# Kernel optimization log

Measured on AMD Instinct MI355X. Metric: run time of the kernel, lower is better.

The kernel has to match this reference:

```python
import jax, jax.numpy as jnp
import numpy as np

N, D = 16384, 16     # nodes (hits), node feature dim (= embedding dim, slice is full)
K = 64               # max_num_neighbors
MAX_RADIUS = 6.0     # kNN radius cut
PID_MAX = 5000


def setup_inputs() -> dict:
    key = jax.random.key(0)
    k1, k2 = jax.random.split(key)
    x = jax.random.normal(k1, (N, D), dtype=jnp.float32)
    particle_id = jax.random.randint(k2, (N,), 0, PID_MAX, dtype=jnp.int32)
    return {"x": x, "particle_id": particle_id}


def reference(x, particle_id):
    # ml is None and embedding_slice=(None,None) -> embedding features are x itself
    emb = x
    # knn_graph: squared pairwise distances, self-loops excluded (diag = +inf)
    sq = jnp.sum(emb * emb, axis=1)                       # [N]
    d2 = sq[:, None] + sq[None, :] - 2.0 * (emb @ emb.T)  # [N, N]
    diag = jnp.arange(N)
    d2 = d2.at[diag, diag].set(jnp.inf)
    _, nbr = jax.lax.top_k(-d2, K)                        # [N, K] nearest neighbor ids
    src = nbr.reshape(-1)                                 # edge_index[0]: neighbor (source)
    dst = jnp.repeat(jnp.arange(N, dtype=src.dtype), K)   # edge_index[1]: query node
    # radius filter: keep edges with dist < max_radius (fixed shape -> boolean mask)
    diff = x[src] - x[dst]                                # [N*K, D]
    dists = jnp.sqrt(jnp.maximum(jnp.sum(diff * diff, axis=1), 0.0))
    mask = dists < MAX_RADIUS                             # [N*K]
    # edge truth labels: same (nonzero) particle id on both ends
    y = (particle_id[src] == particle_id[dst]) & (particle_id[src] > 0) & mask
    # edge features: [x_src - x_dst, x_src + x_dst], zeroed on masked-out edges
    edge_features = jnp.concatenate([diff, x[src] + x[dst]], axis=1)
    edge_features = edge_features * mask[:, None].astype(x.dtype)
    edge_index = jnp.stack([src, dst])                    # [2, N*K]
    return x, edge_index, y.astype(jnp.int32), edge_features, mask
```

## Files before the change

kernel.cpp:

```cpp
#include <hip/hip_runtime.h>

#define NN 16384
#define DD 16
#define KK 64
#define QQ 4
#define TPB 256
#define HIST 1024
#define HISTW (HIST/2)
#define LIST_MAX 768
#define CAND_MAX 256

__device__ __forceinline__ float halving_sumsq16(const float* v) {
    float p[16];
#pragma unroll
    for (int d = 0; d < 16; ++d) p[d] = __fmul_rn(v[d], v[d]);
    float r8[8];
#pragma unroll
    for (int j = 0; j < 8; ++j) r8[j] = __fadd_rn(p[j], p[j + 8]);
    float r4[4];
#pragma unroll
    for (int j = 0; j < 4; ++j) r4[j] = __fadd_rn(r8[j], r8[j + 4]);
    float r2[2];
#pragma unroll
    for (int j = 0; j < 2; ++j) r2[j] = __fadd_rn(r4[j], r4[j + 2]);
    return __fadd_rn(r2[0], r2[1]);
}

__device__ __forceinline__ float d2_of(const float* xi, const float* xj,
                                       float sqi, float sqj) {
    float dot = 0.0f;
#pragma unroll
    for (int d = 0; d < DD; ++d) dot = fmaf(xi[d], xj[d], dot);
    return __fsub_rn(__fadd_rn(sqi, sqj), __fmul_rn(2.0f, dot));
}

__device__ __forceinline__ int bucket_of(float d2) {
    int b = (int)__fmul_rn(d2, 4.0f);
    if (b < 0) b = 0;
    if (b >= HIST) b = HIST - 1;
    return b;
}

#define LOAD_XQ()                                                              \
    float xq[QQ][DD];                                                          \
    float sq[QQ], Tq[QQ];                                                      \
    _Pragma("unroll") for (int q = 0; q < QQ; ++q) {                           \
        const float4* p = reinterpret_cast<const float4*>(x + (iA + q) * DD);  \
        float4 a0 = p[0], a1 = p[1], a2 = p[2], a3 = p[3];                     \
        xq[q][0]=a0.x; xq[q][1]=a0.y; xq[q][2]=a0.z; xq[q][3]=a0.w;            \
        xq[q][4]=a1.x; xq[q][5]=a1.y; xq[q][6]=a1.z; xq[q][7]=a1.w;            \
        xq[q][8]=a2.x; xq[q][9]=a2.y; xq[q][10]=a2.z; xq[q][11]=a2.w;          \
        xq[q][12]=a3.x; xq[q][13]=a3.y; xq[q][14]=a3.z; xq[q][15]=a3.w;        \
        sq[q] = sqf[iA + q];                                                   \
        Tq[q] = 16.0f + sq[q] - 1.8f * sqrtf(32.0f + 4.0f * sq[q]);            \
    }

#define LOAD_XJ(j)                                                             \
    const float4* xj4 = reinterpret_cast<const float4*>(x + (j) * DD);         \
    float4 a0 = xj4[0], a1 = xj4[1], a2 = xj4[2], a3 = xj4[3];                 \
    float xj[DD] = {a0.x, a0.y, a0.z, a0.w, a1.x, a1.y, a1.z, a1.w,            \
                    a2.x, a2.y, a2.z, a2.w, a3.x, a3.y, a3.z, a3.w};

__global__ void prep_kernel(const float* __restrict__ x,
                            float* __restrict__ out_x,
                            float* __restrict__ sqf) {
    int i = blockIdx.x * blockDim.x + threadIdx.x;
    if (i < NN) {
        float v[DD];
#pragma unroll
        for (int d = 0; d < DD; ++d) v[d] = x[i * DD + d];
        sqf[i] = halving_sumsq16(v);
    }
    for (int t = i; t < NN * DD; t += gridDim.x * blockDim.x) {
        out_x[t] = x[t];
    }
}

__global__ __launch_bounds__(TPB) void scan_kernel(
        const float* __restrict__ x,
        const float* __restrict__ sqf,
        unsigned int* __restrict__ ws_cnt,
        unsigned short* __restrict__ ws_list) {
    __shared__ unsigned short list[QQ][LIST_MAX];
    __shared__ unsigned int s_cnt[QQ];

    const int bid = blockIdx.x;
    const int tid = threadIdx.x;
    const int lane = tid & 63;
    const int iA = bid * QQ;

    if (tid < QQ) s_cnt[tid] = 0;
    LOAD_XQ();
    __syncthreads();

    for (int j = tid; j < NN; j += TPB) {
        LOAD_XJ(j);
        const float sj = sqf[j];
#pragma unroll
        for (int q = 0; q < QQ; ++q) {
            float d2 = d2_of(xq[q], xj, sq[q], sj);
            bool want = d2 < Tq[q];
            unsigned long long m = __ballot(want);
            if (want) {
                int leader = __ffsll(m) - 1;
                unsigned int base = 0;
                if (lane == leader)
                    base = atomicAdd(&s_cnt[q], (unsigned int)__popcll(m));
                base = __shfl(base, leader, 64);
                unsigned int pos =
                    base + (unsigned int)__popcll(m & ((1ull << lane) - 1ull));
                if (pos < LIST_MAX) list[q][pos] = (unsigned short)j;
            }
        }
    }
    __syncthreads();

    for (int q = 0; q < QQ; ++q) {
        int lc = (int)min(s_cnt[q], (unsigned int)LIST_MAX);
        unsigned short* dst = ws_list + ((long)iA + q) * LIST_MAX;
        for (int e = tid; e < lc; e += TPB) dst[e] = list[q][e];
    }
    if (tid < QQ) ws_cnt[iA + tid] = s_cnt[tid];
}

__global__ __launch_bounds__(TPB) void select_kernel(
        const float* __restrict__ x,
        const int* __restrict__ pid,
        const float* __restrict__ sqf,
        const unsigned int* __restrict__ ws_cnt,
        const unsigned short* __restrict__ ws_list,
        float* __restrict__ out_src,
        float* __restrict__ out_dst,
        float* __restrict__ out_y,
        float* __restrict__ out_ef,
        float* __restrict__ out_mask) {
    __shared__ unsigned short list[QQ][LIST_MAX];
    __shared__ unsigned int hist[QQ][HISTW];
    __shared__ unsigned int cand_key[QQ][CAND_MAX];
    __shared__ int cand_idx[QQ][CAND_MAX];
    __shared__ unsigned int wavesum[QQ][TPB / 64];
    __shared__ int s_bsel[QQ];
    __shared__ unsigned int s_excnt[QQ], s_candcnt[QQ], s_lc[QQ];
    __shared__ int s_fb[QQ];

    const int bid = blockIdx.x;
    const int tid = threadIdx.x;
    const int lane = tid & 63;
    const int w = tid >> 6;
    const int iA = bid * QQ;

    for (int t = tid; t < QQ * HISTW; t += TPB)
        ((unsigned int*)hist)[t] = 0;
    if (tid < QQ) {
        s_excnt[tid] = 0; s_candcnt[tid] = 0; s_bsel[tid] = HIST - 1;
        s_lc[tid] = min(ws_cnt[iA + tid], (unsigned int)LIST_MAX);
    }
    LOAD_XQ();
    __syncthreads();

    for (int q = 0; q < QQ; ++q) {
        const unsigned short* src = ws_list + ((long)iA + q) * LIST_MAX;
        const int lc = (int)s_lc[q];
        for (int e = tid; e < lc; e += TPB) list[q][e] = src[e];
    }
    __syncthreads();

    for (int q = 0; q < QQ; ++q) {
        const int lc = (int)s_lc[q];
        unsigned int my = 0;
        for (int e = tid; e < lc; e += TPB) {
            const int j = list[q][e];
            LOAD_XJ(j);
            float d2 = d2_of(xq[q], xj, sq[q], sqf[j]);
            my += (d2 < Tq[q]) ? 1u : 0u;
            int b = bucket_of(d2);
            atomicAdd(&hist[q][b >> 1], 1u << ((b & 1) << 4));
        }
        unsigned int v = my;
#pragma unroll
        for (int off = 1; off < 64; off <<= 1) v += __shfl_xor(v, off, 64);
        if (lane == 0 && v) atomicAdd(&s_excnt[q], v);
    }
    __syncthreads();

    if (tid < QQ)
        s_fb[tid] = (ws_cnt[iA + tid] > LIST_MAX) || (s_excnt[tid] < KK + 1);
    __syncthreads();
    const int anyfb = s_fb[0] | s_fb[1] | s_fb[2] | s_fb[3];

    if (anyfb) {
#pragma unroll
        for (int q = 0; q < QQ; ++q)
            if (s_fb[q])
                for (int t = tid; t < HISTW; t += TPB) hist[q][t] = 0;
        __syncthreads();
        for (int j = tid; j < NN; j += TPB) {
            LOAD_XJ(j);
            const float sj = sqf[j];
#pragma unroll
            for (int q = 0; q < QQ; ++q) {
                if (s_fb[q] && j != iA + q) {
                    float d2 = d2_of(xq[q], xj, sq[q], sj);
                    int b = bucket_of(d2);
                    atomicAdd(&hist[q][b >> 1], 1u << ((b & 1) << 4));
                }
            }
        }
    }
    __syncthreads();

    {
        unsigned int local[QQ], inc[QQ];
        unsigned int pc0[QQ], pc1[QQ], pc2[QQ], pc3[QQ];
#pragma unroll
        for (int q = 0; q < QQ; ++q) {
            unsigned int h0 = hist[q][2 * tid];
            unsigned int h1 = hist[q][2 * tid + 1];
            pc0[q] = h0 & 0xFFFFu; pc1[q] = h0 >> 16;
            pc2[q] = h1 & 0xFFFFu; pc3[q] = h1 >> 16;
            unsigned int s = pc0[q] + pc1[q] + pc2[q] + pc3[q];
            local[q] = s;
            unsigned int v = s;
#pragma unroll
            for (int off = 1; off < 64; off <<= 1) {
                unsigned int n = __shfl_up(v, off, 64);
                if (lane >= off) v += n;
            }
            inc[q] = v;
        }
        if (lane == 63)
#pragma unroll
            for (int q = 0; q < QQ; ++q) wavesum[q][w] = inc[q];
        __syncthreads();
#pragma unroll
        for (int q = 0; q < QQ; ++q) {
            const unsigned int need = s_fb[q] ? KK : (KK + 1);
            unsigned int woff = 0;
            for (int ww = 0; ww < w; ++ww) woff += wavesum[q][ww];
            unsigned int cum = inc[q] + woff;
            unsigned int prev = cum - local[q];
            if (prev < need && need <= cum) {
                unsigned int acc = prev;
                int b = 4 * tid;
                if (acc + pc0[q] < need) { acc += pc0[q]; ++b;
                    if (acc + pc1[q] < need) { acc += pc1[q]; ++b;
                        if (acc + pc2[q] < need) { acc += pc2[q]; ++b; } } }
                s_bsel[q] = b;
            }
        }
    }
    __syncthreads();

#pragma unroll
    for (int q = 0; q < QQ; ++q) {
        if (!s_fb[q]) {
            const int bsel = s_bsel[q];
            const int lc = (int)s_lc[q];
            for (int e = tid; e < lc; e += TPB) {
                const int j = list[q][e];
                LOAD_XJ(j);
                float d2 = d2_of(xq[q], xj, sq[q], sqf[j]);
                if (bucket_of(d2) <= bsel && j != iA + q) {
                    unsigned int pos = atomicAdd(&s_candcnt[q], 1u);
                    if (pos < CAND_MAX) {
                        unsigned int u = __float_as_uint(d2);
                        u ^= (u & 0x80000000u) ? 0xFFFFFFFFu : 0x80000000u;
                        cand_key[q][pos] = u;
                        cand_idx[q][pos] = j;
                    }
                }
            }
        }
    }
    if (anyfb) {
        for (int j = tid; j < NN; j += TPB) {
            LOAD_XJ(j);
            const float sj = sqf[j];
#pragma unroll
            for (int q = 0; q < QQ; ++q) {
                if (s_fb[q] && j != iA + q) {
                    float d2 = d2_of(xq[q], xj, sq[q], sj);
                    if (bucket_of(d2) <= s_bsel[q]) {
                        unsigned int pos = atomicAdd(&s_candcnt[q], 1u);
                        if (pos < CAND_MAX) {
                            unsigned int u = __float_as_uint(d2);
                            u ^= (u & 0x80000000u) ? 0xFFFFFFFFu : 0x80000000u;
                            cand_key[q][pos] = u;
                            cand_idx[q][pos] = j;
                        }
                    }
                }
            }
        }
    }
    __syncthreads();

    for (int q = 0; q < QQ; ++q) {
        const int iq = iA + q;
        const int mypid = pid[iq];
        int c = (int)s_candcnt[q];
        if (c > CAND_MAX) c = CAND_MAX;
        for (int t = tid; t < c; t += TPB) {
            const unsigned int kt = cand_key[q][t];
            const int jt = cand_idx[q][t];
            int rank = 0;
            for (int u = 0; u < c; ++u) {
                unsigned int ku = cand_key[q][u];
                rank += (ku < kt) || (ku == kt && cand_idx[q][u] < jt);
            }
            if (rank < KK) {
                const long e = (long)iq * KK + rank;
                out_src[e] = (float)jt;

                const float* xjp = x + jt * DD;
                float diff[DD], sum[DD];
#pragma unroll
                for (int d = 0; d < DD; ++d) {
                    float a = xjp[d], b = xq[q][d];
                    diff[d] = __fsub_rn(a, b);
                    sum[d]  = __fadd_rn(a, b);
                }
                const float s2 = halving_sumsq16(diff);
                const bool m = __fsqrt_rn(s2) < 6.0f;
                out_mask[e] = m ? 1.0f : 0.0f;
                const int pj = pid[jt];
                out_y[e] = (m && pj == mypid && pj > 0) ? 1.0f : 0.0f;

                float* ef = out_ef + e * (2 * DD);
#pragma unroll
                for (int d = 0; d < DD; ++d) ef[d] = m ? diff[d] : 0.0f;
#pragma unroll
                for (int d = 0; d < DD; ++d) ef[DD + d] = m ? sum[d] : 0.0f;
            }
        }
    }

    for (int t = tid; t < QQ * KK; t += TPB) {
        out_dst[(long)iA * KK + t] = (float)(iA + t / KK);
    }
}

extern "C" void kernel_launch(void* const* d_in, const int* in_sizes, int n_in,
                              void* d_out, int out_size, void* d_ws, size_t ws_size,
                              hipStream_t stream) {
    const float* x = (const float*)d_in[0];
    const int* pid = (const int*)d_in[1];
    float* out = (float*)d_out;

    float* out_x   = out;
    float* out_src = out_x + NN * DD;
    float* out_dst = out_src + NN * KK;
    float* out_y   = out_dst + NN * KK;
    float* out_ef  = out_y + NN * KK;
    float* out_mask = out_ef + (long)NN * KK * 2 * DD;

    float* sqf = (float*)d_ws;
    unsigned int* ws_cnt = (unsigned int*)((char*)d_ws + NN * sizeof(float));
    unsigned short* ws_list =
        (unsigned short*)((char*)d_ws + NN * sizeof(float) + NN * sizeof(unsigned int));

    prep_kernel<<<NN / 256, 256, 0, stream>>>(x, out_x, sqf);
    scan_kernel<<<NN / QQ, TPB, 0, stream>>>(x, sqf, ws_cnt, ws_list);
    select_kernel<<<NN / QQ, TPB, 0, stream>>>(x, pid, sqf, ws_cnt, ws_list,
                                               out_src, out_dst, out_y,
                                               out_ef, out_mask);
}
```

Before: 426.5 us.

## Replace per-iteration ballot/atomic list append with bitmask plus prefix-scan compaction

```diff
diff --git a/kernel.cpp b/kernel.cpp
--- a/kernel.cpp
+++ b/kernel.cpp
@@ -5,6 +5,7 @@
 #define KK 64
 #define QQ 4
 #define TPB 256
+#define NCHUNK 8
 #define HIST 1024
 #define HISTW (HIST/2)
 #define LIST_MAX 768
@@ -82,45 +83,86 @@
         unsigned int* __restrict__ ws_cnt,
         unsigned short* __restrict__ ws_list) {
     __shared__ unsigned short list[QQ][LIST_MAX];
-    __shared__ unsigned int s_cnt[QQ];
+    __shared__ unsigned int wcnt[TPB / 64][QQ];
+    __shared__ unsigned int s_listcnt[QQ];
 
     const int bid = blockIdx.x;
     const int tid = threadIdx.x;
     const int lane = tid & 63;
+    const int w = tid >> 6;
     const int iA = bid * QQ;
 
-    if (tid < QQ) s_cnt[tid] = 0;
     LOAD_XQ();
-    __syncthreads();
-
-    for (int j = tid; j < NN; j += TPB) {
-        LOAD_XJ(j);
-        const float sj = sqf[j];
+
+    unsigned int w32s[NCHUNK];
+#pragma unroll
+    for (int c = 0; c < NCHUNK; ++c) {
+        unsigned int bits = 0;
+#pragma unroll
+        for (int k = 0; k < 8; ++k) {
+            const int j = (c * 8 + k) * TPB + tid;
+            LOAD_XJ(j);
+            const float sj = sqf[j];
+#pragma unroll
+            for (int q = 0; q < QQ; ++q) {
+                float d2 = d2_of(xq[q], xj, sq[q], sj);
+                if (d2 < Tq[q]) bits |= (1u << (4 * k + q));
+            }
+        }
+        w32s[c] = bits;
+    }
+
+    {
+        unsigned int cnt[QQ] = {0, 0, 0, 0};
+#pragma unroll
+        for (int c = 0; c < NCHUNK; ++c)
+#pragma unroll
+            for (int q = 0; q < QQ; ++q)
+                cnt[q] += (unsigned int)__popc(w32s[c] & (0x11111111u << q));
+        unsigned int excl[QQ];
 #pragma unroll
         for (int q = 0; q < QQ; ++q) {
-            float d2 = d2_of(xq[q], xj, sq[q], sj);
-            bool want = d2 < Tq[q];
-            unsigned long long m = __ballot(want);
-            if (want) {
-                int leader = __ffsll(m) - 1;
-                unsigned int base = 0;
-                if (lane == leader)
-                    base = atomicAdd(&s_cnt[q], (unsigned int)__popcll(m));
-                base = __shfl(base, leader, 64);
-                unsigned int pos =
-                    base + (unsigned int)__popcll(m & ((1ull << lane) - 1ull));
-                if (pos < LIST_MAX) list[q][pos] = (unsigned short)j;
+            unsigned int v = cnt[q];
+#pragma unroll
+            for (int off = 1; off < 64; off <<= 1) {
+                unsigned int n = __shfl_up(v, off, 64);
+                if (lane >= off) v += n;
+            }
+            excl[q] = v - cnt[q];
+            if (lane == 63) wcnt[w][q] = v;
+        }
+        __syncthreads();
+        if (tid < QQ)
+            s_listcnt[tid] = wcnt[0][tid] + wcnt[1][tid] + wcnt[2][tid] + wcnt[3][tid];
+        unsigned int cur[QQ];
+#pragma unroll
+        for (int q = 0; q < QQ; ++q) {
+            unsigned int b = 0;
+            for (int ww = 0; ww < w; ++ww) b += wcnt[ww][q];
+            cur[q] = b + excl[q];
+        }
+#pragma unroll
+        for (int c = 0; c < NCHUNK; ++c) {
+            unsigned int t32 = w32s[c];
+            while (t32) {
+                int b = __ffs(t32) - 1;
+                int q = b & 3;
+                int k = b >> 2;
+                unsigned int pos = cur[q]++;
+                if (pos < LIST_MAX)
+                    list[q][pos] = (unsigned short)((c * 8 + k) * TPB + tid);
+                t32 &= t32 - 1;
             }
         }
     }
     __syncthreads();
 
     for (int q = 0; q < QQ; ++q) {
-        int lc = (int)min(s_cnt[q], (unsigned int)LIST_MAX);
+        int lc = (int)min(s_listcnt[q], (unsigned int)LIST_MAX);
         unsigned short* dst = ws_list + ((long)iA + q) * LIST_MAX;
         for (int e = tid; e < lc; e += TPB) dst[e] = list[q][e];
     }
-    if (tid < QQ) ws_cnt[iA + tid] = s_cnt[tid];
+    if (tid < QQ) ws_cnt[iA + tid] = s_listcnt[tid];
 }
 
 __global__ __launch_bounds__(TPB) void select_kernel(
```

Result: slower. 733.4 us (+71.9%).

## Replace scalar candidate scan with bf16 MFMA distance scan and bitmask compaction

Applied to the files above, without the earlier changes.

```diff
diff --git a/kernel.cpp b/kernel.cpp
--- a/kernel.cpp
+++ b/kernel.cpp
@@ -4,11 +4,16 @@
 #define DD 16
 #define KK 64
 #define QQ 4
+#define QS 16
 #define TPB 256
 #define HIST 1024
 #define HISTW (HIST/2)
 #define LIST_MAX 768
 #define CAND_MAX 256
+#define EPS 1.5f
+
+typedef __attribute__((ext_vector_type(8))) short s16x8;
+typedef __attribute__((ext_vector_type(4))) float f32x4;
 
 __device__ __forceinline__ float halving_sumsq16(const float* v) {
     float p[16];
@@ -39,6 +44,10 @@
     if (b < 0) b = 0;
     if (b >= HIST) b = HIST - 1;
     return b;
+}
+
+__device__ __forceinline__ float tq_of(float sq) {
+    return 16.0f + sq - 2.0f * sqrtf(32.0f + 4.0f * sq);
 }
 
 #define LOAD_XQ()                                                              \
@@ -52,7 +61,7 @@
         xq[q][8]=a2.x; xq[q][9]=a2.y; xq[q][10]=a2.z; xq[q][11]=a2.w;          \
         xq[q][12]=a3.x; xq[q][13]=a3.y; xq[q][14]=a3.z; xq[q][15]=a3.w;        \
         sq[q] = sqf[iA + q];                                                   \
-        Tq[q] = 16.0f + sq[q] - 1.8f * sqrtf(32.0f + 4.0f * sq[q]);            \
+        Tq[q] = tq_of(sq[q]);                                                  \
     }
 
 #define LOAD_XJ(j)                                                             \
@@ -63,64 +72,101 @@
 
 __global__ void prep_kernel(const float* __restrict__ x,
                             float* __restrict__ out_x,
-                            float* __restrict__ sqf) {
+                            float* __restrict__ sqf,
+                            unsigned short* __restrict__ xbf) {
     int i = blockIdx.x * blockDim.x + threadIdx.x;
     if (i < NN) {
         float v[DD];
 #pragma unroll
         for (int d = 0; d < DD; ++d) v[d] = x[i * DD + d];
         sqf[i] = halving_sumsq16(v);
+#pragma unroll
+        for (int d = 0; d < DD; ++d) {
+            unsigned int u = __float_as_uint(v[d]);
+            xbf[i * DD + d] =
+                (unsigned short)((u + 0x7FFFu + ((u >> 16) & 1u)) >> 16);
+        }
     }
     for (int t = i; t < NN * DD; t += gridDim.x * blockDim.x) {
         out_x[t] = x[t];
     }
 }
 
-__global__ __launch_bounds__(TPB) void scan_kernel(
-        const float* __restrict__ x,
+__global__ __launch_bounds__(TPB) void mfma_scan_kernel(
+        const unsigned short* __restrict__ xbf,
         const float* __restrict__ sqf,
         unsigned int* __restrict__ ws_cnt,
         unsigned short* __restrict__ ws_list) {
-    __shared__ unsigned short list[QQ][LIST_MAX];
-    __shared__ unsigned int s_cnt[QQ];
-
-    const int bid = blockIdx.x;
+    __shared__ unsigned long long bm[16][TPB];
+    __shared__ unsigned int wcnt[4][QS];
+
     const int tid = threadIdx.x;
     const int lane = tid & 63;
-    const int iA = bid * QQ;
-
-    if (tid < QQ) s_cnt[tid] = 0;
-    LOAD_XQ();
-    __syncthreads();
-
-    for (int j = tid; j < NN; j += TPB) {
-        LOAD_XJ(j);
-        const float sj = sqf[j];
-#pragma unroll
-        for (int q = 0; q < QQ; ++q) {
-            float d2 = d2_of(xq[q], xj, sq[q], sj);
-            bool want = d2 < Tq[q];
-            unsigned long long m = __ballot(want);
-            if (want) {
-                int leader = __ffsll(m) - 1;
-                unsigned int base = 0;
-                if (lane == leader)
-                    base = atomicAdd(&s_cnt[q], (unsigned int)__popcll(m));
-                base = __shfl(base, leader, 64);
-                unsigned int pos =
-                    base + (unsigned int)__popcll(m & ((1ull << lane) - 1ull));
-                if (pos < LIST_MAX) list[q][pos] = (unsigned short)j;
-            }
-        }
-    }
-    __syncthreads();
-
-    for (int q = 0; q < QQ; ++q) {
-        int lc = (int)min(s_cnt[q], (unsigned int)LIST_MAX);
-        unsigned short* dst = ws_list + ((long)iA + q) * LIST_MAX;
-        for (int e = tid; e < lc; e += TPB) dst[e] = list[q][e];
-    }
-    if (tid < QQ) ws_cnt[iA + tid] = s_cnt[tid];
+    const int w = tid >> 6;
+    const int qsel = lane & 15;
+    const int grp = lane >> 4;
+    const int iA = blockIdx.x * QS;
+
+    const float sqq = sqf[iA + qsel];
+    const float thr = tq_of(sqq) + EPS;
+
+    s16x8 bq = (s16x8)0;
+    if (grp < 2)
+        bq = *reinterpret_cast<const s16x8*>(xbf + (iA + qsel) * DD + 8 * grp);
+
+    for (int ww = 0; ww < 16; ++ww) {
+        unsigned long long acc = 0ull;
+        for (int tt = 0; tt < 16; ++tt) {
+            const int t = w * 256 + ww * 16 + tt;
+            s16x8 aj = (s16x8)0;
+            if (grp < 2)
+                aj = *reinterpret_cast<const s16x8*>(
+                    xbf + (t * 16 + qsel) * DD + 8 * grp);
+            f32x4 c = {0.f, 0.f, 0.f, 0.f};
+            c = __builtin_amdgcn_mfma_f32_16x16x32_bf16(aj, bq, c, 0, 0, 0);
+            float4 sjv = reinterpret_cast<const float4*>(sqf)[t * 4 + grp];
+            unsigned int nib = 0;
+            if ((sqq + sjv.x) - 2.0f * c[0] < thr) nib |= 1u;
+            if ((sqq + sjv.y) - 2.0f * c[1] < thr) nib |= 2u;
+            if ((sqq + sjv.z) - 2.0f * c[2] < thr) nib |= 4u;
+            if ((sqq + sjv.w) - 2.0f * c[3] < thr) nib |= 8u;
+            acc |= ((unsigned long long)nib) << (4 * tt);
+        }
+        bm[ww][tid] = acc;
+    }
+    __syncthreads();
+
+    unsigned int cnt = 0;
+    for (int ww = 0; ww < 16; ++ww) cnt += (unsigned int)__popcll(bm[ww][tid]);
+    unsigned int v = cnt;
+#pragma unroll
+    for (int off = 16; off <= 32; off <<= 1) {
+        unsigned int n = __shfl_up(v, off, 64);
+        if (lane >= off) v += n;
+    }
+    const unsigned int excl = v - cnt;
+    if (grp == 3) wcnt[w][qsel] = v;
+    __syncthreads();
+
+    unsigned int base = 0;
+    for (int ww2 = 0; ww2 < w; ++ww2) base += wcnt[ww2][qsel];
+    unsigned int cur = base + excl;
+
+    if (tid < QS)
+        ws_cnt[iA + tid] = wcnt[0][tid] + wcnt[1][tid] + wcnt[2][tid] + wcnt[3][tid];
+
+    unsigned short* dst = ws_list + (long)(iA + qsel) * LIST_MAX;
+    for (int ww = 0; ww < 16; ++ww) {
+        unsigned long long m64 = bm[ww][tid];
+        while (m64) {
+            int b = __ffsll(m64) - 1;
+            int tt = b >> 2, r = b & 3;
+            int j = (w * 256 + ww * 16 + tt) * 16 + grp * 4 + r;
+            if (cur < LIST_MAX) dst[cur] = (unsigned short)j;
+            ++cur;
+            m64 &= m64 - 1;
+        }
+    }
 }
 
 __global__ __launch_bounds__(TPB) void select_kernel(
@@ -354,13 +400,15 @@
     float* out_ef  = out_y + NN * KK;
     float* out_mask = out_ef + (long)NN * KK * 2 * DD;
 
-    float* sqf = (float*)d_ws;
-    unsigned int* ws_cnt = (unsigned int*)((char*)d_ws + NN * sizeof(float));
+    char* wsb = (char*)d_ws;
+    float* sqf = (float*)wsb;
+    unsigned short* xbf = (unsigned short*)(wsb + (long)NN * 4);
+    unsigned int* ws_cnt = (unsigned int*)(wsb + (long)NN * 4 + (long)NN * DD * 2);
     unsigned short* ws_list =
-        (unsigned short*)((char*)d_ws + NN * sizeof(float) + NN * sizeof(unsigned int));
-
-    prep_kernel<<<NN / 256, 256, 0, stream>>>(x, out_x, sqf);
-    scan_kernel<<<NN / QQ, TPB, 0, stream>>>(x, sqf, ws_cnt, ws_list);
+        (unsigned short*)(wsb + (long)NN * 4 + (long)NN * DD * 2 + (long)NN * 4);
+
+    prep_kernel<<<NN / 256, 256, 0, stream>>>(x, out_x, sqf, xbf);
+    mfma_scan_kernel<<<NN / QS, TPB, 0, stream>>>(xbf, sqf, ws_cnt, ws_list);
     select_kernel<<<NN / QQ, TPB, 0, stream>>>(x, pid, sqf, ws_cnt, ws_list,
                                                out_src, out_dst, out_y,
                                                out_ef, out_mask);
```

New measurement: 482.6 us. 1.13x slower.
